# Kernel tuning notes

Hardware: AMD Instinct MI355X
Metric: run time of the kernel (lower is better)

The kernel has to match this reference:

```python
import jax, jax.numpy as jnp
import numpy as np

NEG_SLOPE = 0.2
EPS = 1e-16  # PyG softmax denominator epsilon


def gat_conv(x, src, dst, W, a_src, a_dst, bias, concat):
    """PyG-style GATConv (eval mode, self-loops already included in src/dst)."""
    H, D = a_src.shape
    N = x.shape[0]
    h = (x @ W).reshape(N, H, D)                     # [N,H,D]
    alpha_s = jnp.einsum('nhd,hd->nh', h, a_src)     # [N,H]
    alpha_d = jnp.einsum('nhd,hd->nh', h, a_dst)     # [N,H]
    e = alpha_s[src] + alpha_d[dst]                  # [E,H]
    e = jax.nn.leaky_relu(e, NEG_SLOPE)
    # segment softmax over destination nodes
    m = jax.ops.segment_max(e, dst, num_segments=N)  # [N,H]
    m = jax.lax.stop_gradient(m)
    w = jnp.exp(e - m[dst])                          # [E,H]
    denom = jax.ops.segment_sum(w, dst, num_segments=N)  # [N,H]
    a = w / (denom[dst] + EPS)                       # [E,H]
    msg = h[src] * a[:, :, None]                     # [E,H,D]
    out = jax.ops.segment_sum(msg, dst, num_segments=N)  # [N,H,D]
    out = out.reshape(N, H * D) if concat else out.mean(axis=1)
    return out + bias


def setup_inputs() -> dict:
    key = jax.random.key(0)
    ks = jax.random.split(key, 10)
    N, E = 50000, 800000
    F_IN, H, D, C = 256, 4, 64, 64
    HID = H * D  # 256
    x = jax.random.normal(ks[0], (N, F_IN), dtype=jnp.float32)
    edge_index = jax.random.randint(ks[1], (2, E), 0, N, dtype=jnp.int64)
    g = 1.0 / np.sqrt(F_IN)
    W0 = jax.random.normal(ks[2], (F_IN, HID), dtype=jnp.float32) * g
    att_src0 = jax.random.normal(ks[3], (H, D), dtype=jnp.float32) * 0.1
    att_dst0 = jax.random.normal(ks[4], (H, D), dtype=jnp.float32) * 0.1
    b0 = jnp.zeros((HID,), dtype=jnp.float32)
    g2 = 1.0 / np.sqrt(HID)
    W1 = jax.random.normal(ks[5], (HID, C), dtype=jnp.float32) * g2
    att_src1 = jax.random.normal(ks[6], (1, C), dtype=jnp.float32) * 0.1
    att_dst1 = jax.random.normal(ks[7], (1, C), dtype=jnp.float32) * 0.1
    b1 = jnp.zeros((C,), dtype=jnp.float32)
    return {"x": x, "edge_index": edge_index, "W0": W0, "att_src0": att_src0,
            "att_dst0": att_dst0, "b0": b0, "W1": W1, "att_src1": att_src1,
            "att_dst1": att_dst1, "b1": b1}


def reference(x, edge_index, W0, att_src0, att_dst0, b0, W1, att_src1, att_dst1, b1):
    N = x.shape[0]
    loops = jnp.arange(N, dtype=edge_index.dtype)
    src = jnp.concatenate([edge_index[0], loops])  # add self-loops (PyG default)
    dst = jnp.concatenate([edge_index[1], loops])
    # layer 0: concat heads, then ELU (dropout is identity in eval mode)
    h = gat_conv(x, src, dst, W0, att_src0, att_dst0, b0, concat=True)
    h = jax.nn.elu(h)
    # layer 1: single head, no concat (mean over 1 head)
    out = gat_conv(h, src, dst, W1, att_src1, att_dst1, b1, concat=False)
    return out
```

## Files before the change

### kernel.cpp

```cpp
#include <hip/hip_runtime.h>
#include <hip/hip_bf16.h>
#include <math.h>


#define NEG_SLOPE 0.2f
#define CAP0 128
#define CAP1 128

typedef __attribute__((ext_vector_type(8))) short bf16x8;
typedef __attribute__((ext_vector_type(4))) float f32x4;

static __device__ __forceinline__ unsigned f2bf_rne(float f) {
  unsigned u = __float_as_uint(f);
  return (u + 0x7fffu + ((u >> 16) & 1u)) >> 16;
}
static __device__ __forceinline__ float bf2f(unsigned u16) {
  return __uint_as_float(u16 << 16);
}
static __device__ __forceinline__ void fma4(float4& acc, float w, uint2 v) {
  acc.x = fmaf(w, __uint_as_float(v.x << 16), acc.x);
  acc.y = fmaf(w, __uint_as_float(v.x & 0xffff0000u), acc.y);
  acc.z = fmaf(w, __uint_as_float(v.y << 16), acc.z);
  acc.w = fmaf(w, __uint_as_float(v.y & 0xffff0000u), acc.w);
}


__global__ void gat_cvtT_bf16(const float* __restrict__ W,
                              ushort* __restrict__ Wt, int K, int Nw) {
  int i = blockIdx.x * blockDim.x + threadIdx.x;
  if (i >= K * Nw) return;
  int n = i / K, k = i - n * K;
  Wt[i] = (ushort)f2bf_rne(W[(size_t)k * Nw + n]);
}


__global__ void gat_count_kernel(const int* __restrict__ dst, int E, int N,
                                 int* __restrict__ counts) {
  int i = blockIdx.x * blockDim.x + threadIdx.x;
  int ET = E + N;
  if (i >= ET) return;
  int d = (i < E) ? dst[i] : (i - E);
  atomicAdd(&counts[d], 1);
}

__global__ __launch_bounds__(1024) void gat_scan_kernel(
    const int* __restrict__ counts, int* __restrict__ row_off,
    int* __restrict__ cursor, int n) {
  __shared__ int wsum[16];
  __shared__ int s_carry;
  int tid = threadIdx.x;
  int lane = tid & 63;
  int wid = tid >> 6;
  if (tid == 0) s_carry = 0;
  __syncthreads();
  const int TILE = 4096;
  for (int base = 0; base < n; base += TILE) {
    int idx = base + tid * 4;
    int4 v = {0, 0, 0, 0};
    if (idx + 3 < n) {
      v = *(const int4*)&counts[idx];
    } else {
      if (idx + 0 < n) v.x = counts[idx + 0];
      if (idx + 1 < n) v.y = counts[idx + 1];
      if (idx + 2 < n) v.z = counts[idx + 2];
      if (idx + 3 < n) v.w = counts[idx + 3];
    }
    int t0 = v.x, t1 = t0 + v.y, t2 = t1 + v.z, t3 = t2 + v.w;
    int x = t3;
    #pragma unroll
    for (int off = 1; off < 64; off <<= 1) {
      int y = __shfl_up(x, off, 64);
      if (lane >= off) x += y;
    }
    if (lane == 63) wsum[wid] = x;
    __syncthreads();
    if (tid < 16) {
      int s = wsum[tid];
      #pragma unroll
      for (int off = 1; off < 16; off <<= 1) {
        int y = __shfl_up(s, off, 16);
        if (tid >= off) s += y;
      }
      wsum[tid] = s;
    }
    __syncthreads();
    int carry = s_carry;
    int excl_wave = (wid > 0) ? wsum[wid - 1] : 0;
    int b = carry + excl_wave + (x - t3);
    if (idx + 0 < n) { row_off[idx + 0] = b;      cursor[idx + 0] = b;      }
    if (idx + 1 < n) { row_off[idx + 1] = b + t0; cursor[idx + 1] = b + t0; }
    if (idx + 2 < n) { row_off[idx + 2] = b + t1; cursor[idx + 2] = b + t1; }
    if (idx + 3 < n) { row_off[idx + 3] = b + t2; cursor[idx + 3] = b + t2; }
    __syncthreads();
    if (tid == 1023) s_carry = b + t3;
    __syncthreads();
  }
  if (threadIdx.x == 0) row_off[n] = s_carry;
}

__global__ void gat_fill_kernel(const int* __restrict__ src,
                                const int* __restrict__ dst, int E, int N,
                                int* __restrict__ cursor, int* __restrict__ col) {
  int i = blockIdx.x * blockDim.x + threadIdx.x;
  int ET = E + N;
  if (i >= ET) return;
  int s, d;
  if (i < E) { s = src[i]; d = dst[i]; }
  else       { s = d = i - E; }
  int pos = atomicAdd(&cursor[d], 1);
  col[pos] = s;
}


template <int THREADS, int BN, int WM, int WN, bool WRITE_BF16, bool ALPHA,
          bool CVT_A>
__global__ __launch_bounds__(THREADS) void gat_gemm_bf16(
    const float* __restrict__ Af, const ushort* __restrict__ Ab,
    const ushort* __restrict__ Bt, ushort* __restrict__ Cb, int M, int K,
    int N, const float* __restrict__ a_src, const float* __restrict__ a_dst,
    float* __restrict__ as_out, float* __restrict__ ad_out, int H) {
  constexpr int BM = 128, BK = 32;
  constexpr int MR = WM / 16, NR = WN / 16;
  constexpr int WCOLS = BN / WN;
  constexpr int RPP = THREADS / 4;
  static_assert(BM % RPP == 0 && BN % RPP == 0, "staging");
  static_assert((BM / WM) * (BN / WN) == THREADS / 64, "wave tiling");
  __shared__ __align__(16) ushort Al[BM][40];
  __shared__ __align__(16) ushort Bl[BN][40];
  int tid = threadIdx.x;
  int lane = tid & 63, wid = tid >> 6;
  int wrow = (wid / WCOLS) * WM, wcol = (wid % WCOLS) * WN;
  int brow = blockIdx.x * BM, bcol = blockIdx.y * BN;
  int r0 = tid >> 2, seg = tid & 3;
  int kg = lane >> 4, rl = lane & 15;
  f32x4 acc[MR][NR] = {};
  for (int k0 = 0; k0 < K; k0 += BK) {
    #pragma unroll
    for (int h = 0; h < BM / RPP; ++h) {
      int row = r0 + h * RPP;
      int ar = brow + row;
      uint4 v = make_uint4(0u, 0u, 0u, 0u);
      if (ar < M) {
        if constexpr (CVT_A) {
          float4 a0 = *(const float4*)&Af[(size_t)ar * K + k0 + seg * 8];
          float4 a1 = *(const float4*)&Af[(size_t)ar * K + k0 + seg * 8 + 4];
          v.x = f2bf_rne(a0.x) | (f2bf_rne(a0.y) << 16);
          v.y = f2bf_rne(a0.z) | (f2bf_rne(a0.w) << 16);
          v.z = f2bf_rne(a1.x) | (f2bf_rne(a1.y) << 16);
          v.w = f2bf_rne(a1.z) | (f2bf_rne(a1.w) << 16);
        } else {
          v = *(const uint4*)&Ab[(size_t)ar * K + k0 + seg * 8];
        }
      }
      *(uint4*)&Al[row][seg * 8] = v;
    }
    #pragma unroll
    for (int h = 0; h < BN / RPP; ++h) {
      int row = r0 + h * RPP;
      uint4 v = *(const uint4*)&Bt[(size_t)(bcol + row) * K + k0 + seg * 8];
      *(uint4*)&Bl[row][seg * 8] = v;
    }
    __syncthreads();
    bf16x8 af[MR], bfr[NR];
    #pragma unroll
    for (int m = 0; m < MR; ++m)
      af[m] = *(const bf16x8*)&Al[wrow + m * 16 + rl][kg * 8];
    #pragma unroll
    for (int n = 0; n < NR; ++n)
      bfr[n] = *(const bf16x8*)&Bl[wcol + n * 16 + rl][kg * 8];
    #pragma unroll
    for (int m = 0; m < MR; ++m)
      #pragma unroll
      for (int n = 0; n < NR; ++n)
        acc[m][n] = __builtin_amdgcn_mfma_f32_16x16x32_bf16(
            af[m], bfr[n], acc[m][n], 0, 0, 0);
    __syncthreads();
  }
  int orow = kg * 4;
  #pragma unroll
  for (int m = 0; m < MR; ++m) {
    #pragma unroll
    for (int j = 0; j < 4; ++j) {
      int r = brow + wrow + m * 16 + orow + j;
      if (r < M) {
        #pragma unroll
        for (int n = 0; n < NR; ++n) {
          int c = bcol + wcol + n * 16 + rl;
          float v = acc[m][n][j];
          if constexpr (WRITE_BF16) Cb[(size_t)r * N + c] = (ushort)f2bf_rne(v);
        }
      }
    }
  }
  if constexpr (ALPHA) {
    static_assert(WN == 64, "alpha fusion needs one head per wave");
    int hh = (bcol + wcol) >> 6;
    float asv[NR], adv[NR];
    #pragma unroll
    for (int n = 0; n < NR; ++n) {
      asv[n] = a_src[hh * 64 + n * 16 + rl];
      adv[n] = a_dst[hh * 64 + n * 16 + rl];
    }
    #pragma unroll
    for (int m = 0; m < MR; ++m) {
      #pragma unroll
      for (int j = 0; j < 4; ++j) {
        float ps = 0.f, pd = 0.f;
        #pragma unroll
        for (int n = 0; n < NR; ++n) {
          ps = fmaf(acc[m][n][j], asv[n], ps);
          pd = fmaf(acc[m][n][j], adv[n], pd);
        }
        #pragma unroll
        for (int off = 1; off < 16; off <<= 1) {
          ps += __shfl_xor(ps, off, 64);
          pd += __shfl_xor(pd, off, 64);
        }
        int r = brow + wrow + m * 16 + orow + j;
        if (rl == 0 && r < M) {
          as_out[(size_t)r * H + hh] = ps;
          ad_out[(size_t)r * H + hh] = pd;
        }
      }
    }
  }
}


__global__ __launch_bounds__(256) void gat_agg0_kernel(
    const unsigned* __restrict__ h0b, const float* __restrict__ as,
    const float* __restrict__ ad, const int* __restrict__ row_off,
    const int* __restrict__ col, const float* __restrict__ bias,
    ushort* __restrict__ x1b, int N) {
  __shared__ int scol[4][CAP0];
  __shared__ float wt[4][CAP0][4];
  int lane = threadIdx.x & 63;
  int wid = threadIdx.x >> 6;
  int n = blockIdx.x * 4 + wid;
  if (n >= N) return;
  int beg = row_off[n];
  int deg = row_off[n + 1] - beg;
  int degc = deg < CAP0 ? deg : CAP0;
  for (int jj = lane; jj < degc; jj += 64) scol[wid][jj] = col[beg + jj];

  int q = lane >> 4, slot = lane & 15;
  float adv = ad[n * 4 + q];

  float m = -INFINITY;
  for (int jj = slot; jj < deg; jj += 16) {
    int s = (jj < CAP0) ? scol[wid][jj] : col[beg + jj];
    float e = as[s * 4 + q] + adv;
    e = (e > 0.f) ? e : NEG_SLOPE * e;
    if (jj < CAP0) wt[wid][jj][q] = e;
    m = fmaxf(m, e);
  }
  #pragma unroll
  for (int off = 8; off; off >>= 1) m = fmaxf(m, __shfl_xor(m, off, 64));

  float dsum = 0.f;
  for (int jj = slot; jj < deg; jj += 16) {
    float e;
    if (jj < CAP0) {
      e = wt[wid][jj][q];
    } else {
      int s = col[beg + jj];
      e = as[s * 4 + q] + adv;
      e = (e > 0.f) ? e : NEG_SLOPE * e;
    }
    float w = __expf(e - m);
    if (jj < CAP0) wt[wid][jj][q] = w;
    dsum += w;
  }
  #pragma unroll
  for (int off = 8; off; off >>= 1) dsum += __shfl_xor(dsum, off, 64);
  float inv = 1.f / (dsum + 1e-16f);

  float4 acc = make_float4(0.f, 0.f, 0.f, 0.f);
  int c2 = lane * 2;
  if (deg <= CAP0) {
    int jj = 0;
    for (; jj + 4 <= deg; jj += 4) {
      int s0 = __builtin_amdgcn_readfirstlane(scol[wid][jj + 0]);
      int s1 = __builtin_amdgcn_readfirstlane(scol[wid][jj + 1]);
      int s2 = __builtin_amdgcn_readfirstlane(scol[wid][jj + 2]);
      int s3 = __builtin_amdgcn_readfirstlane(scol[wid][jj + 3]);
      uint2 v0 = *(const uint2*)(h0b + (size_t)s0 * 128 + c2);
      uint2 v1 = *(const uint2*)(h0b + (size_t)s1 * 128 + c2);
      uint2 v2 = *(const uint2*)(h0b + (size_t)s2 * 128 + c2);
      uint2 v3 = *(const uint2*)(h0b + (size_t)s3 * 128 + c2);
      float w0 = wt[wid][jj + 0][q];
      float w1 = wt[wid][jj + 1][q];
      float w2 = wt[wid][jj + 2][q];
      float w3 = wt[wid][jj + 3][q];
      fma4(acc, w0, v0); fma4(acc, w1, v1);
      fma4(acc, w2, v2); fma4(acc, w3, v3);
    }
    for (; jj < deg; ++jj) {
      int s = __builtin_amdgcn_readfirstlane(scol[wid][jj]);
      uint2 v = *(const uint2*)(h0b + (size_t)s * 128 + c2);
      fma4(acc, wt[wid][jj][q], v);
    }
  } else {
    for (int jj = 0; jj < deg; ++jj) {
      int s = (jj < CAP0) ? scol[wid][jj] : col[beg + jj];
      s = __builtin_amdgcn_readfirstlane(s);
      uint2 v = *(const uint2*)(h0b + (size_t)s * 128 + c2);
      float w;
      if (jj < CAP0) {
        w = wt[wid][jj][q];
      } else {
        float e = as[s * 4 + q] + adv;
        e = (e > 0.f) ? e : NEG_SLOPE * e;
        w = __expf(e - m);
      }
      fma4(acc, w, v);
    }
  }

  int c0 = lane * 4;
  float4 bv = *(const float4*)&bias[c0];
  float o0 = acc.x * inv + bv.x;
  float o1 = acc.y * inv + bv.y;
  float o2 = acc.z * inv + bv.z;
  float o3 = acc.w * inv + bv.w;
  o0 = (o0 > 0.f) ? o0 : (__expf(o0) - 1.f);
  o1 = (o1 > 0.f) ? o1 : (__expf(o1) - 1.f);
  o2 = (o2 > 0.f) ? o2 : (__expf(o2) - 1.f);
  o3 = (o3 > 0.f) ? o3 : (__expf(o3) - 1.f);
  uint2 p;
  p.x = f2bf_rne(o0) | (f2bf_rne(o1) << 16);
  p.y = f2bf_rne(o2) | (f2bf_rne(o3) << 16);
  *(uint2*)&x1b[(size_t)n * 256 + c0] = p;
}


__global__ __launch_bounds__(256) void gat_agg1_kernel(
    const ushort* __restrict__ h1b, const float* __restrict__ as,
    const float* __restrict__ ad, const int* __restrict__ row_off,
    const int* __restrict__ col, const float* __restrict__ bias,
    float* __restrict__ out, int N) {
  __shared__ int scol[4][CAP1];
  __shared__ float wt[4][CAP1];
  int lane = threadIdx.x & 63;
  int wid = threadIdx.x >> 6;
  int n = blockIdx.x * 4 + wid;
  if (n >= N) return;
  int beg = row_off[n];
  int deg = row_off[n + 1] - beg;
  int degc = deg < CAP1 ? deg : CAP1;
  for (int jj = lane; jj < degc; jj += 64) scol[wid][jj] = col[beg + jj];
  float adv = ad[n];

  float m = -INFINITY;
  for (int jj = lane; jj < deg; jj += 64) {
    int s = (jj < CAP1) ? scol[wid][jj] : col[beg + jj];
    float e = as[s] + adv;
    e = (e > 0.f) ? e : NEG_SLOPE * e;
    if (jj < CAP1) wt[wid][jj] = e;
    m = fmaxf(m, e);
  }
  #pragma unroll
  for (int off = 32; off; off >>= 1) m = fmaxf(m, __shfl_xor(m, off, 64));

  float dsum = 0.f;
  for (int jj = lane; jj < deg; jj += 64) {
    float e;
    if (jj < CAP1) {
      e = wt[wid][jj];
    } else {
      int s = col[beg + jj];
      e = as[s] + adv;
      e = (e > 0.f) ? e : NEG_SLOPE * e;
    }
    float w = __expf(e - m);
    if (jj < CAP1) wt[wid][jj] = w;
    dsum += w;
  }
  #pragma unroll
  for (int off = 32; off; off >>= 1) dsum += __shfl_xor(dsum, off, 64);
  float inv = 1.f / (dsum + 1e-16f);

  int half = lane >> 5, c = lane & 31;
  float ax = 0.f, ay = 0.f;
  if (deg <= CAP1) {
    int Pf = deg >> 1;
    int t = 0;
    for (; t + 4 <= Pf; t += 4) {
      int j0 = 2 * t + half;
      int s0 = scol[wid][j0 + 0];
      int s1 = scol[wid][j0 + 2];
      int s2 = scol[wid][j0 + 4];
      int s3 = scol[wid][j0 + 6];
      unsigned v0 = *(const unsigned*)(h1b + (size_t)s0 * 64 + c * 2);
      unsigned v1 = *(const unsigned*)(h1b + (size_t)s1 * 64 + c * 2);
      unsigned v2 = *(const unsigned*)(h1b + (size_t)s2 * 64 + c * 2);
      unsigned v3 = *(const unsigned*)(h1b + (size_t)s3 * 64 + c * 2);
      float w0 = wt[wid][j0 + 0];
      float w1 = wt[wid][j0 + 2];
      float w2 = wt[wid][j0 + 4];
      float w3 = wt[wid][j0 + 6];
      ax = fmaf(w0, bf2f(v0 & 0xffffu), ax);
      ay = fmaf(w0, bf2f(v0 >> 16), ay);
      ax = fmaf(w1, bf2f(v1 & 0xffffu), ax);
      ay = fmaf(w1, bf2f(v1 >> 16), ay);
      ax = fmaf(w2, bf2f(v2 & 0xffffu), ax);
      ay = fmaf(w2, bf2f(v2 >> 16), ay);
      ax = fmaf(w3, bf2f(v3 & 0xffffu), ax);
      ay = fmaf(w3, bf2f(v3 >> 16), ay);
    }
    for (; t < Pf; ++t) {
      int j0 = 2 * t + half;
      int s = scol[wid][j0];
      unsigned v = *(const unsigned*)(h1b + (size_t)s * 64 + c * 2);
      float w = wt[wid][j0];
      ax = fmaf(w, bf2f(v & 0xffffu), ax);
      ay = fmaf(w, bf2f(v >> 16), ay);
    }
    if (deg & 1) {
      int jj = deg - 1;
      int s = scol[wid][jj];
      unsigned v = *(const unsigned*)(h1b + (size_t)s * 64 + c * 2);
      float w = (half == 0) ? wt[wid][jj] : 0.f;
      ax = fmaf(w, bf2f(v & 0xffffu), ax);
      ay = fmaf(w, bf2f(v >> 16), ay);
    }
  } else {
    int P = (deg + 1) >> 1;
    for (int t = 0; t < P; ++t) {
      int jj = 2 * t + half;
      int jc = jj < deg ? jj : (deg - 1);
      int s = (jc < CAP1) ? scol[wid][jc] : col[beg + jc];
      unsigned v = *(const unsigned*)(h1b + (size_t)s * 64 + c * 2);
      float w;
      if (jc < CAP1) {
        w = wt[wid][jc];
      } else {
        float e = as[s] + adv;
        e = (e > 0.f) ? e : NEG_SLOPE * e;
        w = __expf(e - m);
      }
      if (jj >= deg) w = 0.f;
      ax = fmaf(w, bf2f(v & 0xffffu), ax);
      ay = fmaf(w, bf2f(v >> 16), ay);
    }
  }
  ax += __shfl_xor(ax, 32, 64);
  ay += __shfl_xor(ay, 32, 64);
  if (half == 0) {
    float2 bv = *(const float2*)&bias[c * 2];
    float2 o;
    o.x = ax * inv + bv.x;
    o.y = ay * inv + bv.y;
    *(float2*)&out[(size_t)n * 64 + c * 2] = o;
  }
}


extern "C" void kernel_launch(void* const* d_in, const int* in_sizes, int n_in,
                              void* d_out, int out_size, void* d_ws, size_t ws_size,
                              hipStream_t stream) {
  const float* x        = (const float*)d_in[0];
  const int*   eidx     = (const int*)d_in[1];
  const float* W0       = (const float*)d_in[2];
  const float* att_src0 = (const float*)d_in[3];
  const float* att_dst0 = (const float*)d_in[4];
  const float* b0       = (const float*)d_in[5];
  const float* W1       = (const float*)d_in[6];
  const float* att_src1 = (const float*)d_in[7];
  const float* att_dst1 = (const float*)d_in[8];
  const float* b1       = (const float*)d_in[9];
  float* out = (float*)d_out;

  const int F_IN = 256, HID = 256, H = 4, C = 64;
  const int N = in_sizes[0] / F_IN;
  const int E = in_sizes[1] / 2;
  const int ET = E + N;

  const int* src = eidx;
  const int* dst = eidx + E;

  char* w = (char*)d_ws;
  auto take = [&](size_t bytes) {
    char* p = w;
    w += (bytes + 255) & ~(size_t)255;
    return p;
  };
  ushort* W0t     = (ushort*)take((size_t)F_IN * HID * 2);
  ushort* W1t     = (ushort*)take((size_t)HID * C * 2);
  ushort* h0b     = (ushort*)take((size_t)N * HID * 2);
  ushort* x1b     = (ushort*)take((size_t)N * HID * 2);
  ushort* h1b     = (ushort*)take((size_t)N * C * 2);
  float*  as0     = (float*)take((size_t)N * H * 4);
  float*  ad0     = (float*)take((size_t)N * H * 4);
  float*  as1     = (float*)take((size_t)N * 4);
  float*  ad1     = (float*)take((size_t)N * 4);
  int*    row_off = (int*)take((size_t)(N + 1) * 4);
  int*    cursor  = (int*)take((size_t)N * 4);
  int*    counts  = (int*)take((size_t)N * 4);
  int*    col     = (int*)take((size_t)ET * 4);

  gat_cvtT_bf16<<<(F_IN * HID + 255) / 256, 256, 0, stream>>>(W0, W0t, F_IN, HID);
  gat_cvtT_bf16<<<(HID * C + 255) / 256, 256, 0, stream>>>(W1, W1t, HID, C);

  (void)hipMemsetAsync(counts, 0, (size_t)N * 4, stream);
  {
    int blocks = (ET + 255) / 256;
    gat_count_kernel<<<blocks, 256, 0, stream>>>(dst, E, N, counts);
    gat_scan_kernel<<<1, 1024, 0, stream>>>(counts, row_off, cursor, N);
    gat_fill_kernel<<<blocks, 256, 0, stream>>>(src, dst, E, N, cursor, col);
  }

  {
    dim3 grid((N + 127) / 128, HID / 256);
    gat_gemm_bf16<512, 256, 64, 64, true, true, true>
        <<<grid, 512, 0, stream>>>(x, nullptr, W0t, h0b, N, F_IN, HID,
                                   att_src0, att_dst0, as0, ad0, H);
  }
  gat_agg0_kernel<<<(N + 3) / 4, 256, 0, stream>>>((const unsigned*)h0b, as0,
                                                   ad0, row_off, col, b0, x1b, N);

  {
    dim3 grid((N + 127) / 128, C / 64);
    gat_gemm_bf16<256, 64, 32, 64, true, true, false>
        <<<grid, 256, 0, stream>>>(nullptr, x1b, W1t, h1b, N, HID, C,
                                   att_src1, att_dst1, as1, ad1, 1);
  }
  gat_agg1_kernel<<<(N + 3) / 4, 256, 0, stream>>>(h1b, as1, ad1, row_off, col,
                                                   b1, out, N);
}
```

Before: 266.6 us.

## Split layer-0 aggregation into softmax pass and per-head sliced gather

```diff
diff --git a/kernel.cpp b/kernel.cpp
--- a/kernel.cpp
+++ b/kernel.cpp
@@ -113,7 +113,7 @@
 
 
 template <int THREADS, int BN, int WM, int WN, bool WRITE_BF16, bool ALPHA,
-          bool CVT_A>
+          bool CVT_A, bool SLICED>
 __global__ __launch_bounds__(THREADS) void gat_gemm_bf16(
     const float* __restrict__ Af, const ushort* __restrict__ Ab,
     const ushort* __restrict__ Bt, ushort* __restrict__ Cb, int M, int K,
@@ -187,7 +187,13 @@
         for (int n = 0; n < NR; ++n) {
           int c = bcol + wcol + n * 16 + rl;
           float v = acc[m][n][j];
-          if constexpr (WRITE_BF16) Cb[(size_t)r * N + c] = (ushort)f2bf_rne(v);
+          if constexpr (WRITE_BF16) {
+            if constexpr (SLICED)
+              Cb[((size_t)(c >> 6) * M + r) * 64 + (c & 63)] =
+                  (ushort)f2bf_rne(v);
+            else
+              Cb[(size_t)r * N + c] = (ushort)f2bf_rne(v);
+          }
         }
       }
     }
@@ -227,11 +233,10 @@
 }
 
 
-__global__ __launch_bounds__(256) void gat_agg0_kernel(
-    const unsigned* __restrict__ h0b, const float* __restrict__ as,
-    const float* __restrict__ ad, const int* __restrict__ row_off,
-    const int* __restrict__ col, const float* __restrict__ bias,
-    ushort* __restrict__ x1b, int N) {
+__global__ __launch_bounds__(256) void gat_sm0_kernel(
+    const float* __restrict__ as, const float* __restrict__ ad,
+    const int* __restrict__ row_off, const int* __restrict__ col,
+    float* __restrict__ wq, int N, int ET) {
   __shared__ int scol[4][CAP0];
   __shared__ float wt[4][CAP0][4];
   int lane = threadIdx.x & 63;
@@ -275,62 +280,111 @@
   for (int off = 8; off; off >>= 1) dsum += __shfl_xor(dsum, off, 64);
   float inv = 1.f / (dsum + 1e-16f);
 
+  for (int jj = slot; jj < deg; jj += 16) {
+    float w;
+    if (jj < CAP0) {
+      w = wt[wid][jj][q];
+    } else {
+      int s = col[beg + jj];
+      float e = as[s * 4 + q] + adv;
+      e = (e > 0.f) ? e : NEG_SLOPE * e;
+      w = __expf(e - m);
+    }
+    wq[(size_t)q * ET + beg + jj] = w * inv;
+  }
+}
+
+
+__global__ __launch_bounds__(256) void gat_agg0s_kernel(
+    const ushort* __restrict__ h0s, const float* __restrict__ wq,
+    const int* __restrict__ row_off, const int* __restrict__ col,
+    const float* __restrict__ bias, ushort* __restrict__ x1b, int N, int ET) {
+  __shared__ int scol[4][CAP0];
+  int lane = threadIdx.x & 63;
+  int wid = threadIdx.x >> 6;
+  int s = blockIdx.x & 3;
+  int g = blockIdx.x >> 2;
+  int n = g * 4 + wid;
+  if (n >= N) return;
+  int beg = row_off[n];
+  int deg = row_off[n + 1] - beg;
+  int degc = deg < CAP0 ? deg : CAP0;
+  for (int jj = lane; jj < degc; jj += 64) scol[wid][jj] = col[beg + jj];
+
+  const float* wqn = wq + (size_t)s * ET + beg;
+  int gidx = lane >> 4, cpos = lane & 15;
+  const ushort* tbl = h0s + (size_t)s * N * 64 + cpos * 4;
+
   float4 acc = make_float4(0.f, 0.f, 0.f, 0.f);
-  int c2 = lane * 2;
   if (deg <= CAP0) {
-    int jj = 0;
-    for (; jj + 4 <= deg; jj += 4) {
-      int s0 = __builtin_amdgcn_readfirstlane(scol[wid][jj + 0]);
-      int s1 = __builtin_amdgcn_readfirstlane(scol[wid][jj + 1]);
-      int s2 = __builtin_amdgcn_readfirstlane(scol[wid][jj + 2]);
-      int s3 = __builtin_amdgcn_readfirstlane(scol[wid][jj + 3]);
-      uint2 v0 = *(const uint2*)(h0b + (size_t)s0 * 128 + c2);
-      uint2 v1 = *(const uint2*)(h0b + (size_t)s1 * 128 + c2);
-      uint2 v2 = *(const uint2*)(h0b + (size_t)s2 * 128 + c2);
-      uint2 v3 = *(const uint2*)(h0b + (size_t)s3 * 128 + c2);
-      float w0 = wt[wid][jj + 0][q];
-      float w1 = wt[wid][jj + 1][q];
-      float w2 = wt[wid][jj + 2][q];
-      float w3 = wt[wid][jj + 3][q];
+    int QF = deg >> 2;
+    int t = 0;
+    for (; t + 4 <= QF; t += 4) {
+      int j0 = 4 * t + gidx;
+      int s0 = scol[wid][j0 + 0];
+      int s1 = scol[wid][j0 + 4];
+      int s2 = scol[wid][j0 + 8];
+      int s3 = scol[wid][j0 + 12];
+      uint2 v0 = *(const uint2*)(tbl + (size_t)s0 * 64);
+      uint2 v1 = *(const uint2*)(tbl + (size_t)s1 * 64);
+      uint2 v2 = *(const uint2*)(tbl + (size_t)s2 * 64);
+      uint2 v3 = *(const uint2*)(tbl + (size_t)s3 * 64);
+      float w0 = wqn[j0 + 0];
+      float w1 = wqn[j0 + 4];
+      float w2 = wqn[j0 + 8];
+      float w3 = wqn[j0 + 12];
       fma4(acc, w0, v0); fma4(acc, w1, v1);
       fma4(acc, w2, v2); fma4(acc, w3, v3);
     }
-    for (; jj < deg; ++jj) {
-      int s = __builtin_amdgcn_readfirstlane(scol[wid][jj]);
-      uint2 v = *(const uint2*)(h0b + (size_t)s * 128 + c2);
-      fma4(acc, wt[wid][jj][q], v);
+    for (; t < QF; ++t) {
+      int j = 4 * t + gidx;
+      int ss = scol[wid][j];
+      uint2 v = *(const uint2*)(tbl + (size_t)ss * 64);
+      fma4(acc, wqn[j], v);
+    }
+    if (deg & 3) {
+      int j = 4 * QF + gidx;
+      int jc = j < deg ? j : deg - 1;
+      int ss = scol[wid][jc];
+      uint2 v = *(const uint2*)(tbl + (size_t)ss * 64);
+      float w = (j < deg) ? wqn[j] : 0.f;
+      fma4(acc, w, v);
     }
   } else {
-    for (int jj = 0; jj < deg; ++jj) {
-      int s = (jj < CAP0) ? scol[wid][jj] : col[beg + jj];
-      s = __builtin_amdgcn_readfirstlane(s);
-      uint2 v = *(const uint2*)(h0b + (size_t)s * 128 + c2);
-      float w;
-      if (jj < CAP0) {
-        w = wt[wid][jj][q];
-      } else {
-        float e = as[s * 4 + q] + adv;
-        e = (e > 0.f) ? e : NEG_SLOPE * e;
-        w = __expf(e - m);
-      }
+    int Q = (deg + 3) >> 2;
+    for (int t = 0; t < Q; ++t) {
+      int j = 4 * t + gidx;
+      int jc = j < deg ? j : deg - 1;
+      int ss = (jc < CAP0) ? scol[wid][jc] : col[beg + jc];
+      uint2 v = *(const uint2*)(tbl + (size_t)ss * 64);
+      float w = (j < deg) ? wqn[j] : 0.f;
       fma4(acc, w, v);
     }
   }
-
-  int c0 = lane * 4;
-  float4 bv = *(const float4*)&bias[c0];
-  float o0 = acc.x * inv + bv.x;
-  float o1 = acc.y * inv + bv.y;
-  float o2 = acc.z * inv + bv.z;
-  float o3 = acc.w * inv + bv.w;
-  o0 = (o0 > 0.f) ? o0 : (__expf(o0) - 1.f);
-  o1 = (o1 > 0.f) ? o1 : (__expf(o1) - 1.f);
-  o2 = (o2 > 0.f) ? o2 : (__expf(o2) - 1.f);
-  o3 = (o3 > 0.f) ? o3 : (__expf(o3) - 1.f);
-  uint2 p;
-  p.x = f2bf_rne(o0) | (f2bf_rne(o1) << 16);
-  p.y = f2bf_rne(o2) | (f2bf_rne(o3) << 16);
-  *(uint2*)&x1b[(size_t)n * 256 + c0] = p;
+  acc.x += __shfl_xor(acc.x, 16, 64);
+  acc.y += __shfl_xor(acc.y, 16, 64);
+  acc.z += __shfl_xor(acc.z, 16, 64);
+  acc.w += __shfl_xor(acc.w, 16, 64);
+  acc.x += __shfl_xor(acc.x, 32, 64);
+  acc.y += __shfl_xor(acc.y, 32, 64);
+  acc.z += __shfl_xor(acc.z, 32, 64);
+  acc.w += __shfl_xor(acc.w, 32, 64);
+  if (gidx == 0) {
+    int ch = s * 64 + cpos * 4;
+    float4 bv = *(const float4*)&bias[ch];
+    float o0 = acc.x + bv.x;
+    float o1 = acc.y + bv.y;
+    float o2 = acc.z + bv.z;
+    float o3 = acc.w + bv.w;
+    o0 = (o0 > 0.f) ? o0 : (__expf(o0) - 1.f);
+    o1 = (o1 > 0.f) ? o1 : (__expf(o1) - 1.f);
+    o2 = (o2 > 0.f) ? o2 : (__expf(o2) - 1.f);
+    o3 = (o3 > 0.f) ? o3 : (__expf(o3) - 1.f);
+    uint2 p;
+    p.x = f2bf_rne(o0) | (f2bf_rne(o1) << 16);
+    p.y = f2bf_rne(o2) | (f2bf_rne(o3) << 16);
+    *(uint2*)&x1b[(size_t)n * 256 + ch] = p;
+  }
 }
 
 
@@ -487,9 +541,10 @@
   };
   ushort* W0t     = (ushort*)take((size_t)F_IN * HID * 2);
   ushort* W1t     = (ushort*)take((size_t)HID * C * 2);
-  ushort* h0b     = (ushort*)take((size_t)N * HID * 2);
+  ushort* h0s     = (ushort*)take((size_t)N * HID * 2);
   ushort* x1b     = (ushort*)take((size_t)N * HID * 2);
   ushort* h1b     = (ushort*)take((size_t)N * C * 2);
+  float*  wq      = (float*)take((size_t)H * ET * 4);
   float*  as0     = (float*)take((size_t)N * H * 4);
   float*  ad0     = (float*)take((size_t)N * H * 4);
   float*  as1     = (float*)take((size_t)N * 4);
@@ -512,16 +567,18 @@
 
   {
     dim3 grid((N + 127) / 128, HID / 256);
-    gat_gemm_bf16<512, 256, 64, 64, true, true, true>
-        <<<grid, 512, 0, stream>>>(x, nullptr, W0t, h0b, N, F_IN, HID,
+    gat_gemm_bf16<512, 256, 64, 64, true, true, true, true>
+        <<<grid, 512, 0, stream>>>(x, nullptr, W0t, h0s, N, F_IN, HID,
                                    att_src0, att_dst0, as0, ad0, H);
   }
-  gat_agg0_kernel<<<(N + 3) / 4, 256, 0, stream>>>((const unsigned*)h0b, as0,
-                                                   ad0, row_off, col, b0, x1b, N);
+  gat_sm0_kernel<<<(N + 3) / 4, 256, 0, stream>>>(as0, ad0, row_off, col, wq,
+                                                  N, ET);
+  gat_agg0s_kernel<<<((N + 3) / 4) * 4, 256, 0, stream>>>(h0s, wq, row_off,
+                                                          col, b0, x1b, N, ET);
 
   {
     dim3 grid((N + 127) / 128, C / 64);
-    gat_gemm_bf16<256, 64, 32, 64, true, true, false>
+    gat_gemm_bf16<256, 64, 32, 64, true, true, false, false>
         <<<grid, 256, 0, stream>>>(nullptr, x1b, W1t, h1b, N, HID, C,
                                    att_src1, att_dst1, as1, ad1, 1);
   }
```

Measured after the change: 313.8 us. 1.18x slower.

## Split layer-0 features into two column slices and aggregate each in separate blocks

Applied to the files above, without the earlier changes.

```diff
diff --git a/kernel.cpp b/kernel.cpp
--- a/kernel.cpp
+++ b/kernel.cpp
@@ -113,7 +113,7 @@
 
 
 template <int THREADS, int BN, int WM, int WN, bool WRITE_BF16, bool ALPHA,
-          bool CVT_A>
+          bool CVT_A, bool SLICED>
 __global__ __launch_bounds__(THREADS) void gat_gemm_bf16(
     const float* __restrict__ Af, const ushort* __restrict__ Ab,
     const ushort* __restrict__ Bt, ushort* __restrict__ Cb, int M, int K,
@@ -187,7 +187,13 @@
         for (int n = 0; n < NR; ++n) {
           int c = bcol + wcol + n * 16 + rl;
           float v = acc[m][n][j];
-          if constexpr (WRITE_BF16) Cb[(size_t)r * N + c] = (ushort)f2bf_rne(v);
+          if constexpr (WRITE_BF16) {
+            if constexpr (SLICED)
+              Cb[((size_t)(c >> 7) * M + r) * 128 + (c & 127)] =
+                  (ushort)f2bf_rne(v);
+            else
+              Cb[(size_t)r * N + c] = (ushort)f2bf_rne(v);
+          }
         }
       }
     }
@@ -228,109 +234,135 @@
 
 
 __global__ __launch_bounds__(256) void gat_agg0_kernel(
-    const unsigned* __restrict__ h0b, const float* __restrict__ as,
+    const ushort* __restrict__ h0s, const float* __restrict__ as,
     const float* __restrict__ ad, const int* __restrict__ row_off,
     const int* __restrict__ col, const float* __restrict__ bias,
     ushort* __restrict__ x1b, int N) {
   __shared__ int scol[4][CAP0];
-  __shared__ float wt[4][CAP0][4];
+  __shared__ float wt[4][CAP0][2];
   int lane = threadIdx.x & 63;
   int wid = threadIdx.x >> 6;
-  int n = blockIdx.x * 4 + wid;
+  int slice = blockIdx.x & 1;
+  int n = (blockIdx.x >> 1) * 4 + wid;
   if (n >= N) return;
   int beg = row_off[n];
   int deg = row_off[n + 1] - beg;
   int degc = deg < CAP0 ? deg : CAP0;
   for (int jj = lane; jj < degc; jj += 64) scol[wid][jj] = col[beg + jj];
 
-  int q = lane >> 4, slot = lane & 15;
-  float adv = ad[n * 4 + q];
+  int q2 = lane >> 5;
+  int qh = slice * 2 + q2;
+  int slot = lane & 31;
+  float adv = ad[n * 4 + qh];
 
   float m = -INFINITY;
-  for (int jj = slot; jj < deg; jj += 16) {
+  for (int jj = slot; jj < deg; jj += 32) {
     int s = (jj < CAP0) ? scol[wid][jj] : col[beg + jj];
-    float e = as[s * 4 + q] + adv;
+    float e = as[s * 4 + qh] + adv;
     e = (e > 0.f) ? e : NEG_SLOPE * e;
-    if (jj < CAP0) wt[wid][jj][q] = e;
+    if (jj < CAP0) wt[wid][jj][q2] = e;
     m = fmaxf(m, e);
   }
   #pragma unroll
-  for (int off = 8; off; off >>= 1) m = fmaxf(m, __shfl_xor(m, off, 64));
+  for (int off = 16; off; off >>= 1) m = fmaxf(m, __shfl_xor(m, off, 64));
 
   float dsum = 0.f;
-  for (int jj = slot; jj < deg; jj += 16) {
+  for (int jj = slot; jj < deg; jj += 32) {
     float e;
     if (jj < CAP0) {
-      e = wt[wid][jj][q];
+      e = wt[wid][jj][q2];
     } else {
       int s = col[beg + jj];
-      e = as[s * 4 + q] + adv;
+      e = as[s * 4 + qh] + adv;
       e = (e > 0.f) ? e : NEG_SLOPE * e;
     }
     float w = __expf(e - m);
-    if (jj < CAP0) wt[wid][jj][q] = w;
+    if (jj < CAP0) wt[wid][jj][q2] = w;
     dsum += w;
   }
   #pragma unroll
-  for (int off = 8; off; off >>= 1) dsum += __shfl_xor(dsum, off, 64);
+  for (int off = 16; off; off >>= 1) dsum += __shfl_xor(dsum, off, 64);
   float inv = 1.f / (dsum + 1e-16f);
+  float m0 = __shfl(m, 0, 64), m1 = __shfl(m, 32, 64);
+  float i0 = __shfl(inv, 0, 64), i1 = __shfl(inv, 32, 64);
+
+  int eg = lane >> 5;
+  int cpos = lane & 31;
+  int hloc = cpos >> 4;
+  const ushort* tbl = h0s + (size_t)slice * N * 128 + cpos * 4;
 
   float4 acc = make_float4(0.f, 0.f, 0.f, 0.f);
-  int c2 = lane * 2;
   if (deg <= CAP0) {
-    int jj = 0;
-    for (; jj + 4 <= deg; jj += 4) {
-      int s0 = __builtin_amdgcn_readfirstlane(scol[wid][jj + 0]);
-      int s1 = __builtin_amdgcn_readfirstlane(scol[wid][jj + 1]);
-      int s2 = __builtin_amdgcn_readfirstlane(scol[wid][jj + 2]);
-      int s3 = __builtin_amdgcn_readfirstlane(scol[wid][jj + 3]);
-      uint2 v0 = *(const uint2*)(h0b + (size_t)s0 * 128 + c2);
-      uint2 v1 = *(const uint2*)(h0b + (size_t)s1 * 128 + c2);
-      uint2 v2 = *(const uint2*)(h0b + (size_t)s2 * 128 + c2);
-      uint2 v3 = *(const uint2*)(h0b + (size_t)s3 * 128 + c2);
-      float w0 = wt[wid][jj + 0][q];
-      float w1 = wt[wid][jj + 1][q];
-      float w2 = wt[wid][jj + 2][q];
-      float w3 = wt[wid][jj + 3][q];
+    int Pf = deg >> 1;
+    int t = 0;
+    for (; t + 4 <= Pf; t += 4) {
+      int j0 = 2 * t + eg;
+      int s0 = scol[wid][j0 + 0];
+      int s1 = scol[wid][j0 + 2];
+      int s2 = scol[wid][j0 + 4];
+      int s3 = scol[wid][j0 + 6];
+      uint2 v0 = *(const uint2*)(tbl + (size_t)s0 * 128);
+      uint2 v1 = *(const uint2*)(tbl + (size_t)s1 * 128);
+      uint2 v2 = *(const uint2*)(tbl + (size_t)s2 * 128);
+      uint2 v3 = *(const uint2*)(tbl + (size_t)s3 * 128);
+      float w0 = wt[wid][j0 + 0][hloc];
+      float w1 = wt[wid][j0 + 2][hloc];
+      float w2 = wt[wid][j0 + 4][hloc];
+      float w3 = wt[wid][j0 + 6][hloc];
       fma4(acc, w0, v0); fma4(acc, w1, v1);
       fma4(acc, w2, v2); fma4(acc, w3, v3);
     }
-    for (; jj < deg; ++jj) {
-      int s = __builtin_amdgcn_readfirstlane(scol[wid][jj]);
-      uint2 v = *(const uint2*)(h0b + (size_t)s * 128 + c2);
-      fma4(acc, wt[wid][jj][q], v);
+    for (; t < Pf; ++t) {
+      int j0 = 2 * t + eg;
+      int s = scol[wid][j0];
+      uint2 v = *(const uint2*)(tbl + (size_t)s * 128);
+      fma4(acc, wt[wid][j0][hloc], v);
+    }
+    if (deg & 1) {
+      int jj = deg - 1;
+      int s = scol[wid][jj];
+      uint2 v = *(const uint2*)(tbl + (size_t)s * 128);
+      float w = (eg == 0) ? wt[wid][jj][hloc] : 0.f;
+      fma4(acc, w, v);
     }
   } else {
-    for (int jj = 0; jj < deg; ++jj) {
+    float mh = hloc ? m1 : m0;
+    float advh = ad[n * 4 + slice * 2 + hloc];
+    for (int jj = eg; jj < deg; jj += 2) {
       int s = (jj < CAP0) ? scol[wid][jj] : col[beg + jj];
-      s = __builtin_amdgcn_readfirstlane(s);
-      uint2 v = *(const uint2*)(h0b + (size_t)s * 128 + c2);
+      uint2 v = *(const uint2*)(tbl + (size_t)s * 128);
       float w;
       if (jj < CAP0) {
-        w = wt[wid][jj][q];
+        w = wt[wid][jj][hloc];
       } else {
-        float e = as[s * 4 + q] + adv;
+        float e = as[s * 4 + slice * 2 + hloc] + advh;
         e = (e > 0.f) ? e : NEG_SLOPE * e;
-        w = __expf(e - m);
+        w = __expf(e - mh);
       }
       fma4(acc, w, v);
     }
   }
-
-  int c0 = lane * 4;
-  float4 bv = *(const float4*)&bias[c0];
-  float o0 = acc.x * inv + bv.x;
-  float o1 = acc.y * inv + bv.y;
-  float o2 = acc.z * inv + bv.z;
-  float o3 = acc.w * inv + bv.w;
-  o0 = (o0 > 0.f) ? o0 : (__expf(o0) - 1.f);
-  o1 = (o1 > 0.f) ? o1 : (__expf(o1) - 1.f);
-  o2 = (o2 > 0.f) ? o2 : (__expf(o2) - 1.f);
-  o3 = (o3 > 0.f) ? o3 : (__expf(o3) - 1.f);
-  uint2 p;
-  p.x = f2bf_rne(o0) | (f2bf_rne(o1) << 16);
-  p.y = f2bf_rne(o2) | (f2bf_rne(o3) << 16);
-  *(uint2*)&x1b[(size_t)n * 256 + c0] = p;
+  acc.x += __shfl_xor(acc.x, 32, 64);
+  acc.y += __shfl_xor(acc.y, 32, 64);
+  acc.z += __shfl_xor(acc.z, 32, 64);
+  acc.w += __shfl_xor(acc.w, 32, 64);
+  if (eg == 0) {
+    float myinv = hloc ? i1 : i0;
+    int ch = slice * 128 + cpos * 4;
+    float4 bv = *(const float4*)&bias[ch];
+    float o0 = acc.x * myinv + bv.x;
+    float o1 = acc.y * myinv + bv.y;
+    float o2 = acc.z * myinv + bv.z;
+    float o3 = acc.w * myinv + bv.w;
+    o0 = (o0 > 0.f) ? o0 : (__expf(o0) - 1.f);
+    o1 = (o1 > 0.f) ? o1 : (__expf(o1) - 1.f);
+    o2 = (o2 > 0.f) ? o2 : (__expf(o2) - 1.f);
+    o3 = (o3 > 0.f) ? o3 : (__expf(o3) - 1.f);
+    uint2 p;
+    p.x = f2bf_rne(o0) | (f2bf_rne(o1) << 16);
+    p.y = f2bf_rne(o2) | (f2bf_rne(o3) << 16);
+    *(uint2*)&x1b[(size_t)n * 256 + ch] = p;
+  }
 }
 
 
@@ -487,7 +519,7 @@
   };
   ushort* W0t     = (ushort*)take((size_t)F_IN * HID * 2);
   ushort* W1t     = (ushort*)take((size_t)HID * C * 2);
-  ushort* h0b     = (ushort*)take((size_t)N * HID * 2);
+  ushort* h0s     = (ushort*)take((size_t)N * HID * 2);
   ushort* x1b     = (ushort*)take((size_t)N * HID * 2);
   ushort* h1b     = (ushort*)take((size_t)N * C * 2);
   float*  as0     = (float*)take((size_t)N * H * 4);
@@ -512,16 +544,17 @@
 
   {
     dim3 grid((N + 127) / 128, HID / 256);
-    gat_gemm_bf16<512, 256, 64, 64, true, true, true>
-        <<<grid, 512, 0, stream>>>(x, nullptr, W0t, h0b, N, F_IN, HID,
+    gat_gemm_bf16<512, 256, 64, 64, true, true, true, true>
+        <<<grid, 512, 0, stream>>>(x, nullptr, W0t, h0s, N, F_IN, HID,
                                    att_src0, att_dst0, as0, ad0, H);
   }
-  gat_agg0_kernel<<<(N + 3) / 4, 256, 0, stream>>>((const unsigned*)h0b, as0,
-                                                   ad0, row_off, col, b0, x1b, N);
+  gat_agg0_kernel<<<((N + 3) / 4) * 2, 256, 0, stream>>>(h0s, as0, ad0,
+                                                         row_off, col, b0,
+                                                         x1b, N);
 
   {
     dim3 grid((N + 127) / 128, C / 64);
-    gat_gemm_bf16<256, 64, 32, 64, true, true, false>
+    gat_gemm_bf16<256, 64, 32, 64, true, true, false, false>
         <<<grid, 256, 0, stream>>>(nullptr, x1b, W1t, h1b, N, HID, C,
                                    att_src1, att_dst1, as1, ad1, 1);
   }
```

Result: slower. 278.5 us (+4.5%).
